# Kernel tuning notes

Hardware: AMD Instinct MI355X
Metric: run time of the kernel (lower is better)

## Reference

```python
import jax, jax.numpy as jnp
import numpy as np

N_HIT = 50000
N_TRUE = 512
N_EDGE = 40000
D = 8
S_B = 1.0
Q_MIN = 0.5


def setup_inputs() -> dict:
    key = jax.random.key(0)
    k_x, k_f, k_y, k_eh, k_ep = jax.random.split(key, 5)
    x = jax.random.normal(k_x, (N_HIT, D), dtype=jnp.float32)
    # f is a sigmoid-like filter output in (0,1); keep away from 1 so atanh is finite
    f = jax.random.uniform(k_f, (N_HIT,), dtype=jnp.float32, minval=0.01, maxval=0.95)
    # y == -1 marks background hits; otherwise an instance id
    y = jax.random.randint(k_y, (N_HIT,), -1, N_TRUE, dtype=jnp.int64)
    e_h = jax.random.randint(k_eh, (N_EDGE,), 0, N_HIT, dtype=jnp.int64)
    e_p = jax.random.randint(k_ep, (N_EDGE,), 0, N_TRUE, dtype=jnp.int64)
    # guarantee every true particle has at least one assigned hit
    e_p = e_p.at[:N_TRUE].set(jnp.arange(N_TRUE, dtype=jnp.int64))
    return {"x": x, "f": f, "y": y, "e_h": e_h, "e_p": e_p}


def reference(x, f, y, e_h, e_p):
    n_hit = x.shape[0]
    fe = f[e_h]  # [n_edge]
    # scatter_max with zero-initialized output: clamp below at 0
    f_centers = jax.ops.segment_max(fe, e_p, num_segments=N_TRUE)
    f_centers = jnp.maximum(f_centers, 0.0)  # [n_true]
    # argmax hit per particle: among edges attaining the segment max, take largest hit id
    is_max = fe == f_centers[e_p]
    centers = jax.ops.segment_max(jnp.where(is_max, e_h, -1), e_p, num_segments=N_TRUE)  # [n_true]

    bkg_mask = y == -1
    n_bkg = bkg_mask.sum().astype(f.dtype)

    b1 = 1.0 - f_centers.sum() / N_TRUE
    b2 = S_B / n_bkg * jnp.where(bkg_mask, f, 0.0).sum()

    q = jnp.square(jnp.arctanh(f)) + Q_MIN  # [n_hit]

    # membership mask m_ik [n_hit, n_true]
    m_ik = jnp.zeros((n_hit, N_TRUE), dtype=bool).at[e_h, e_p].set(True)

    # pairwise squared distances to condensation centers [n_hit, n_true]
    xc = x[centers]  # [n_true, d]
    dist = jnp.sum(jnp.square(x[:, None, :] - xc[None, :, :]), axis=2)

    # attractive inside instance, hinged repulsive outside
    v = jnp.where(m_ik, dist, jnp.clip(1.0 - dist, 0.0))
    v = (jnp.sum(v * q[centers][None, :], axis=1) * q).sum() / n_hit

    return jnp.stack([b1 + b2, v])
```

## Files before the change

### kernel.cpp

```cpp
#include <hip/hip_runtime.h>
#include <math.h>

#define N_HIT  50000
#define N_TRUE 512
#define N_EDGE 40000
#define Q_MIN  0.5f

#define MASK_WORDS_PER_HIT (N_TRUE / 32)
#define KSPLIT 2
#define KCH (N_TRUE / KSPLIT)
#define HB ((N_HIT + 255) / 256)


__global__ void k_edge_max(const float* __restrict__ f,
                           const int* __restrict__ e_h, const int* __restrict__ e_p,
                           unsigned* __restrict__ fc_bits) {
    int e = blockIdx.x * blockDim.x + threadIdx.x;
    if (e < N_EDGE) {
        float fe = f[e_h[e]];
        atomicMax(&fc_bits[e_p[e]], __float_as_uint(fe));
    }
}

__global__ void k_edge_argmax_mask(const float* __restrict__ f,
                                   const int* __restrict__ e_h, const int* __restrict__ e_p,
                                   const unsigned* __restrict__ fc_bits,
                                   int* __restrict__ centers, unsigned* __restrict__ mask) {
    int e = blockIdx.x * blockDim.x + threadIdx.x;
    if (e < N_EDGE) {
        int h = e_h[e], p = e_p[e];
        if (__float_as_uint(f[h]) == fc_bits[p])
            atomicMax(&centers[p], h);
        atomicOr(&mask[(size_t)h * MASK_WORDS_PER_HIT + (p >> 5)], 1u << (p & 31));
    }
}

__global__ void k_scalars(const float* __restrict__ f, const int* __restrict__ y,
                          const unsigned* __restrict__ fc_bits, const int* __restrict__ centers,
                          float* __restrict__ qc, float* __restrict__ accum) {
    int i = blockIdx.x * blockDim.x + threadIdx.x;
    if (i < N_TRUE) {
        float fc = f[centers[i]];
        float a  = atanhf(fc);
        qc[i] = fmaf(a, a, Q_MIN);
        atomicAdd(&accum[0], __uint_as_float(fc_bits[i]));
    }
    if (i < N_HIT) {
        if (y[i] == -1) {
            atomicAdd(&accum[1], f[i]);
            atomicAdd((unsigned*)&accum[2], 1u);
        }
    }
}

__global__ __launch_bounds__(256) void k_main(const float* __restrict__ x,
                                              const float* __restrict__ f,
                                              const int* __restrict__ centers,
                                              const float* __restrict__ qc,
                                              const unsigned* __restrict__ mask,
                                              float* __restrict__ accum) {
    __shared__ float4 xcs[KCH][2];
    __shared__ float  qcs[KCH];
    __shared__ float  wsum[4];

    int hb = blockIdx.x % HB;
    int kb = blockIdx.x / HB;
    int k0 = kb * KCH;
    int t  = threadIdx.x;

    {
        int c = centers[k0 + t];
        const float4* xp = (const float4*)(x + (size_t)c * 8);
        xcs[t][0] = xp[0];
        xcs[t][1] = xp[1];
        qcs[t]    = qc[k0 + t];
    }
    __syncthreads();

    int   i    = hb * 256 + t;
    float vout = 0.0f;
    if (i < N_HIT) {
        const float4* xp = (const float4*)(x + (size_t)i * 8);
        float4 a0 = xp[0], a1 = xp[1];

        const uint4* mp = (const uint4*)(mask + (size_t)i * MASK_WORDS_PER_HIT + kb * (KCH / 32));
        uint4 m0 = mp[0], m1 = mp[1];
        unsigned mw[8] = {m0.x, m0.y, m0.z, m0.w, m1.x, m1.y, m1.z, m1.w};

        float fi = f[i];
        float at = atanhf(fi);
        float qi = fmaf(at, at, Q_MIN);

        float acc = 0.0f;
#pragma unroll 8
        for (int k = 0; k < KCH; k++) {
            float4 c0 = xcs[k][0], c1 = xcs[k][1];
            float d, dist;
            d = a0.x - c0.x; dist = d * d;
            d = a0.y - c0.y; dist = fmaf(d, d, dist);
            d = a0.z - c0.z; dist = fmaf(d, d, dist);
            d = a0.w - c0.w; dist = fmaf(d, d, dist);
            d = a1.x - c1.x; dist = fmaf(d, d, dist);
            d = a1.y - c1.y; dist = fmaf(d, d, dist);
            d = a1.z - c1.z; dist = fmaf(d, d, dist);
            d = a1.w - c1.w; dist = fmaf(d, d, dist);
            float rep = fmaxf(1.0f - dist, 0.0f);
            bool  mem = (mw[k >> 5] >> (k & 31)) & 1u;
            float sel = mem ? dist : rep;
            acc = fmaf(sel, qcs[k], acc);
        }
        vout = acc * qi;
    }

    for (int off = 32; off > 0; off >>= 1)
        vout += __shfl_down(vout, off, 64);
    if ((t & 63) == 0) wsum[t >> 6] = vout;
    __syncthreads();
    if (t == 0)
        atomicAdd(&accum[3], wsum[0] + wsum[1] + wsum[2] + wsum[3]);
}

__global__ void k_finalize(const float* __restrict__ accum, float* __restrict__ out) {
    if (threadIdx.x == 0 && blockIdx.x == 0) {
        float b1 = 1.0f - accum[0] / (float)N_TRUE;
        unsigned nb = ((const unsigned*)accum)[2];
        float b2 = accum[1] / (float)nb;
        out[0] = b1 + b2;
        out[1] = accum[3] / (float)N_HIT;
    }
}

extern "C" void kernel_launch(void* const* d_in, const int* in_sizes, int n_in,
                              void* d_out, int out_size, void* d_ws, size_t ws_size,
                              hipStream_t stream) {
    const float* x   = (const float*)d_in[0];
    const float* f   = (const float*)d_in[1];
    const int*   y   = (const int*)d_in[2];
    const int*   e_h = (const int*)d_in[3];
    const int*   e_p = (const int*)d_in[4];
    float* out = (float*)d_out;

    unsigned* ws      = (unsigned*)d_ws;
    unsigned* fc_bits = ws;
    int*      centers = (int*)(ws + 512);
    float*    qc      = (float*)(ws + 1024);
    float*    accum   = (float*)(ws + 1536);
    unsigned* mask    = ws + 2048;

    size_t total_bytes = (size_t)(2048 + (size_t)N_HIT * MASK_WORDS_PER_HIT) * 4;
    hipMemsetAsync(d_ws, 0, total_bytes, stream);

    k_edge_max<<<(N_EDGE + 255) / 256, 256, 0, stream>>>(f, e_h, e_p, fc_bits);
    k_edge_argmax_mask<<<(N_EDGE + 255) / 256, 256, 0, stream>>>(f, e_h, e_p, fc_bits, centers, mask);
    k_scalars<<<(N_HIT + 255) / 256, 256, 0, stream>>>(f, y, fc_bits, centers, qc, accum);
    k_main<<<HB * KSPLIT, 256, 0, stream>>>(x, f, centers, qc, mask, accum);
    k_finalize<<<1, 64, 0, stream>>>(accum, out);
}
```

Measured before the change: 109.9 us.

## Restructure pipeline: fused prep/zeroing, LDS segment max, center table, last-block finalize

Replaces the memset plus five kernels with four. The memset is folded into a prep kernel that also computes per-block segment maxima in LDS atomics. The scalar kernel now builds a packed center table (coordinates plus q) and reduces the background sums per block instead of using per-hit global atomics. The main kernel uses 128-thread blocks, reads center data from that global table rather than staging it in LDS, and finalizes through a last-block-done counter with spread partial sums. This aims to cut launch overhead, memset cost and atomic contention, but it relies on cache hits for the center reads inside the inner loop.

```diff
diff --git a/kernel.cpp b/kernel.cpp
--- a/kernel.cpp
+++ b/kernel.cpp
@@ -6,127 +6,175 @@
 #define N_EDGE 40000
 #define Q_MIN  0.5f
 
-#define MASK_WORDS_PER_HIT (N_TRUE / 32)
-#define KSPLIT 2
-#define KCH (N_TRUE / KSPLIT)
-#define HB ((N_HIT + 255) / 256)
+#define W_CENTERS 512
+#define W_SUMFC   1024
+#define W_SUMBKG  1025
+#define W_NBKG    1026
+#define W_DONE    1027
+#define W_VPART   1040
+#define W_ZERO_LO 512
+#define W_ZERO_HI 1168
+#define W_FCPART  2048
+#define W_CTAB    10240
+#define W_MASK    16384
+#define MASK_WPH  16
+#define MASK_U4   (N_HIT * MASK_WPH / 4)
 
+#define A_EDGE_BLOCKS 16
+#define EDGES_PER_BLOCK (N_EDGE / A_EDGE_BLOCKS)
+#define A_GRID 256
 
-__global__ void k_edge_max(const float* __restrict__ f,
-                           const int* __restrict__ e_h, const int* __restrict__ e_p,
-                           unsigned* __restrict__ fc_bits) {
-    int e = blockIdx.x * blockDim.x + threadIdx.x;
-    if (e < N_EDGE) {
-        float fe = f[e_h[e]];
-        atomicMax(&fc_bits[e_p[e]], __float_as_uint(fe));
+#define D_BLOCK 128
+#define D_HB ((N_HIT + D_BLOCK - 1) / D_BLOCK)
+#define D_GRID (D_HB * 2)
+
+__global__ __launch_bounds__(256) void k_prep(const float* __restrict__ f,
+                                              const int* __restrict__ e_h,
+                                              const int* __restrict__ e_p,
+                                              unsigned* __restrict__ ws) {
+    const int b = blockIdx.x, t = threadIdx.x;
+    if (b < A_EDGE_BLOCKS) {
+        __shared__ unsigned lmax[N_TRUE];
+        lmax[t] = 0u; lmax[t + 256] = 0u;
+        __syncthreads();
+        const int e0 = b * EDGES_PER_BLOCK;
+        for (int e = e0 + t; e < e0 + EDGES_PER_BLOCK; e += 256)
+            atomicMax(&lmax[e_p[e]], __float_as_uint(f[e_h[e]]));
+        __syncthreads();
+        ws[W_FCPART + b * N_TRUE + t]       = lmax[t];
+        ws[W_FCPART + b * N_TRUE + t + 256] = lmax[t + 256];
+    } else {
+        const int zb = b - A_EDGE_BLOCKS;
+        if (zb == 0)
+            for (int w = W_ZERO_LO + t; w < W_ZERO_HI; w += 256) ws[w] = 0u;
+        uint4* m4 = (uint4*)(ws + W_MASK);
+        const int nthr = (A_GRID - A_EDGE_BLOCKS) * 256;
+        for (int idx = zb * 256 + t; idx < MASK_U4; idx += nthr)
+            m4[idx] = make_uint4(0u, 0u, 0u, 0u);
     }
 }
 
-__global__ void k_edge_argmax_mask(const float* __restrict__ f,
-                                   const int* __restrict__ e_h, const int* __restrict__ e_p,
-                                   const unsigned* __restrict__ fc_bits,
-                                   int* __restrict__ centers, unsigned* __restrict__ mask) {
-    int e = blockIdx.x * blockDim.x + threadIdx.x;
-    if (e < N_EDGE) {
-        int h = e_h[e], p = e_p[e];
-        if (__float_as_uint(f[h]) == fc_bits[p])
-            atomicMax(&centers[p], h);
-        atomicOr(&mask[(size_t)h * MASK_WORDS_PER_HIT + (p >> 5)], 1u << (p & 31));
-    }
+__global__ __launch_bounds__(256) void k_edge(const float* __restrict__ f,
+                                              const int* __restrict__ e_h,
+                                              const int* __restrict__ e_p,
+                                              unsigned* __restrict__ ws) {
+    const int e = blockIdx.x * 256 + threadIdx.x;
+    if (e >= N_EDGE) return;
+    const int h = e_h[e], p = e_p[e];
+    unsigned fm = 0u;
+#pragma unroll
+    for (int b = 0; b < A_EDGE_BLOCKS; ++b)
+        fm = max(fm, ws[W_FCPART + b * N_TRUE + p]);
+    if (__float_as_uint(f[h]) == fm)
+        atomicMax((int*)ws + W_CENTERS + p, h);
+    atomicOr(&ws[W_MASK + (size_t)h * MASK_WPH + (p >> 5)], 1u << (p & 31));
 }
 
-__global__ void k_scalars(const float* __restrict__ f, const int* __restrict__ y,
-                          const unsigned* __restrict__ fc_bits, const int* __restrict__ centers,
-                          float* __restrict__ qc, float* __restrict__ accum) {
-    int i = blockIdx.x * blockDim.x + threadIdx.x;
-    if (i < N_TRUE) {
-        float fc = f[centers[i]];
-        float a  = atanhf(fc);
-        qc[i] = fmaf(a, a, Q_MIN);
-        atomicAdd(&accum[0], __uint_as_float(fc_bits[i]));
-    }
-    if (i < N_HIT) {
-        if (y[i] == -1) {
-            atomicAdd(&accum[1], f[i]);
-            atomicAdd((unsigned*)&accum[2], 1u);
+__global__ __launch_bounds__(256) void k_scal(const float* __restrict__ x,
+                                              const float* __restrict__ f,
+                                              const int* __restrict__ y,
+                                              unsigned* __restrict__ ws) {
+    const int b = blockIdx.x, t = threadIdx.x;
+    __shared__ float r2[8];
+    if (b == 0) {
+        float local = 0.f;
+        for (int p = t; p < N_TRUE; p += 256) {
+            unsigned fm = 0u;
+#pragma unroll
+            for (int bb = 0; bb < A_EDGE_BLOCKS; ++bb)
+                fm = max(fm, ws[W_FCPART + bb * N_TRUE + p]);
+            local += __uint_as_float(fm);
+            const int c = ((const int*)ws)[W_CENTERS + p];
+            float* ct = (float*)ws + W_CTAB + p * 12;
+            const float4* xp = (const float4*)(x + (size_t)c * 8);
+            ((float4*)ct)[0] = xp[0];
+            ((float4*)ct)[1] = xp[1];
+            const float a = atanhf(f[c]);
+            ct[8] = fmaf(a, a, Q_MIN);
+        }
+        for (int off = 32; off; off >>= 1) local += __shfl_down(local, off, 64);
+        if ((t & 63) == 0) r2[t >> 6] = local;
+        __syncthreads();
+        if (t == 0) ((float*)ws)[W_SUMFC] = r2[0] + r2[1] + r2[2] + r2[3];
+    } else {
+        float sf = 0.f, fc = 0.f;
+        for (int i = (b - 1) * 256 + t; i < N_HIT; i += 16 * 256) {
+            if (y[i] == -1) { sf += f[i]; fc += 1.f; }
+        }
+        for (int off = 32; off; off >>= 1) {
+            sf += __shfl_down(sf, off, 64);
+            fc += __shfl_down(fc, off, 64);
+        }
+        if ((t & 63) == 0) { r2[t >> 6] = sf; r2[4 + (t >> 6)] = fc; }
+        __syncthreads();
+        if (t == 0) {
+            atomicAdd((float*)ws + W_SUMBKG, r2[0] + r2[1] + r2[2] + r2[3]);
+            atomicAdd(&ws[W_NBKG], (unsigned)(r2[4] + r2[5] + r2[6] + r2[7]));
         }
     }
 }
 
-__global__ __launch_bounds__(256) void k_main(const float* __restrict__ x,
-                                              const float* __restrict__ f,
-                                              const int* __restrict__ centers,
-                                              const float* __restrict__ qc,
-                                              const unsigned* __restrict__ mask,
-                                              float* __restrict__ accum) {
-    __shared__ float4 xcs[KCH][2];
-    __shared__ float  qcs[KCH];
-    __shared__ float  wsum[4];
-
-    int hb = blockIdx.x % HB;
-    int kb = blockIdx.x / HB;
-    int k0 = kb * KCH;
-    int t  = threadIdx.x;
-
-    {
-        int c = centers[k0 + t];
-        const float4* xp = (const float4*)(x + (size_t)c * 8);
-        xcs[t][0] = xp[0];
-        xcs[t][1] = xp[1];
-        qcs[t]    = qc[k0 + t];
-    }
-    __syncthreads();
-
-    int   i    = hb * 256 + t;
-    float vout = 0.0f;
+__global__ __launch_bounds__(D_BLOCK) void k_main(const float* __restrict__ x,
+                                                  const float* __restrict__ f,
+                                                  unsigned* __restrict__ ws,
+                                                  float* __restrict__ out) {
+    const int t  = threadIdx.x;
+    const int hb = blockIdx.x >> 1;
+    const int kb = blockIdx.x & 1;
+    const int k0 = kb * 256;
+    const int i  = hb * D_BLOCK + t;
+    const float* ctab = (const float*)ws + W_CTAB;
+    float vout = 0.f;
     if (i < N_HIT) {
         const float4* xp = (const float4*)(x + (size_t)i * 8);
-        float4 a0 = xp[0], a1 = xp[1];
-
-        const uint4* mp = (const uint4*)(mask + (size_t)i * MASK_WORDS_PER_HIT + kb * (KCH / 32));
-        uint4 m0 = mp[0], m1 = mp[1];
-        unsigned mw[8] = {m0.x, m0.y, m0.z, m0.w, m1.x, m1.y, m1.z, m1.w};
-
-        float fi = f[i];
-        float at = atanhf(fi);
-        float qi = fmaf(at, at, Q_MIN);
-
-        float acc = 0.0f;
+        const float4 a0 = xp[0], a1 = xp[1];
+        const float at = atanhf(f[i]);
+        const float qi = fmaf(at, at, Q_MIN);
+        const unsigned* mrow = ws + W_MASK + (size_t)i * MASK_WPH + kb * 8;
+        float acc = 0.f;
+        for (int w = 0; w < 8; ++w) {
+            const unsigned word = mrow[w];
+            const float* ctw = ctab + (size_t)(k0 + w * 32) * 12;
 #pragma unroll 8
-        for (int k = 0; k < KCH; k++) {
-            float4 c0 = xcs[k][0], c1 = xcs[k][1];
-            float d, dist;
-            d = a0.x - c0.x; dist = d * d;
-            d = a0.y - c0.y; dist = fmaf(d, d, dist);
-            d = a0.z - c0.z; dist = fmaf(d, d, dist);
-            d = a0.w - c0.w; dist = fmaf(d, d, dist);
-            d = a1.x - c1.x; dist = fmaf(d, d, dist);
-            d = a1.y - c1.y; dist = fmaf(d, d, dist);
-            d = a1.z - c1.z; dist = fmaf(d, d, dist);
-            d = a1.w - c1.w; dist = fmaf(d, d, dist);
-            float rep = fmaxf(1.0f - dist, 0.0f);
-            bool  mem = (mw[k >> 5] >> (k & 31)) & 1u;
-            float sel = mem ? dist : rep;
-            acc = fmaf(sel, qcs[k], acc);
+            for (int k2 = 0; k2 < 32; ++k2) {
+                const float4 c0 = *(const float4*)(ctw + 12 * k2);
+                const float4 c1 = *(const float4*)(ctw + 12 * k2 + 4);
+                const float qck = ctw[12 * k2 + 8];
+                float d, dist;
+                d = a0.x - c0.x; dist = d * d;
+                d = a0.y - c0.y; dist = fmaf(d, d, dist);
+                d = a0.z - c0.z; dist = fmaf(d, d, dist);
+                d = a0.w - c0.w; dist = fmaf(d, d, dist);
+                d = a1.x - c1.x; dist = fmaf(d, d, dist);
+                d = a1.y - c1.y; dist = fmaf(d, d, dist);
+                d = a1.z - c1.z; dist = fmaf(d, d, dist);
+                d = a1.w - c1.w; dist = fmaf(d, d, dist);
+                const float rep = fmaxf(1.f - dist, 0.f);
+                const float sel = ((word >> k2) & 1u) ? dist : rep;
+                acc = fmaf(sel, qck, acc);
+            }
         }
         vout = acc * qi;
     }
-
-    for (int off = 32; off > 0; off >>= 1)
-        vout += __shfl_down(vout, off, 64);
-    if ((t & 63) == 0) wsum[t >> 6] = vout;
+    for (int off = 32; off; off >>= 1) vout += __shfl_down(vout, off, 64);
+    __shared__ float r[2];
+    if ((t & 63) == 0) r[t >> 6] = vout;
     __syncthreads();
-    if (t == 0)
-        atomicAdd(&accum[3], wsum[0] + wsum[1] + wsum[2] + wsum[3]);
-}
-
-__global__ void k_finalize(const float* __restrict__ accum, float* __restrict__ out) {
-    if (threadIdx.x == 0 && blockIdx.x == 0) {
-        float b1 = 1.0f - accum[0] / (float)N_TRUE;
-        unsigned nb = ((const unsigned*)accum)[2];
-        float b2 = accum[1] / (float)nb;
-        out[0] = b1 + b2;
-        out[1] = accum[3] / (float)N_HIT;
+    if (t == 0) {
+        atomicAdd((float*)ws + W_VPART + (blockIdx.x & 7) * 16, r[0] + r[1]);
+        __threadfence();
+        const unsigned c = atomicAdd(&ws[W_DONE], 1u);
+        if (c == D_GRID - 1) {
+            __threadfence();
+            float vs = 0.f;
+            for (int s = 0; s < 8; ++s)
+                vs += atomicAdd((float*)ws + W_VPART + s * 16, 0.0f);
+            const float sum_fc  = ((const float*)ws)[W_SUMFC];
+            const float sum_bkg = ((const float*)ws)[W_SUMBKG];
+            const float nb = (float)ws[W_NBKG];
+            out[0] = (1.f - sum_fc / (float)N_TRUE) + sum_bkg / nb;
+            out[1] = vs / (float)N_HIT;
+        }
     }
 }
 
@@ -139,20 +187,10 @@
     const int*   e_h = (const int*)d_in[3];
     const int*   e_p = (const int*)d_in[4];
     float* out = (float*)d_out;
+    unsigned* ws = (unsigned*)d_ws;
 
-    unsigned* ws      = (unsigned*)d_ws;
-    unsigned* fc_bits = ws;
-    int*      centers = (int*)(ws + 512);
-    float*    qc      = (float*)(ws + 1024);
-    float*    accum   = (float*)(ws + 1536);
-    unsigned* mask    = ws + 2048;
-
-    size_t total_bytes = (size_t)(2048 + (size_t)N_HIT * MASK_WORDS_PER_HIT) * 4;
-    hipMemsetAsync(d_ws, 0, total_bytes, stream);
-
-    k_edge_max<<<(N_EDGE + 255) / 256, 256, 0, stream>>>(f, e_h, e_p, fc_bits);
-    k_edge_argmax_mask<<<(N_EDGE + 255) / 256, 256, 0, stream>>>(f, e_h, e_p, fc_bits, centers, mask);
-    k_scalars<<<(N_HIT + 255) / 256, 256, 0, stream>>>(f, y, fc_bits, centers, qc, accum);
-    k_main<<<HB * KSPLIT, 256, 0, stream>>>(x, f, centers, qc, mask, accum);
-    k_finalize<<<1, 64, 0, stream>>>(accum, out);
+    k_prep<<<A_GRID, 256, 0, stream>>>(f, e_h, e_p, ws);
+    k_edge<<<(N_EDGE + 255) / 256, 256, 0, stream>>>(f, e_h, e_p, ws);
+    k_scal<<<17, 256, 0, stream>>>(x, f, y, ws);
+    k_main<<<D_GRID, D_BLOCK, 0, stream>>>(x, f, ws, out);
 }
```

Result: slower. 125.2 us (+14.0%).
